# Optimization experiments

Hardware: AMD Instinct MI355X
Metric: run time of the kernel (lower is better)

## Reference

```python
import jax, jax.numpy as jnp
import numpy as np

B, C1, D1, C2, D2 = 128, 1152, 8, 10, 16
ROUTING_ITERS = 3


def squash(s, axis=-1, eps=1e-8):
    # squash(s) = (|s|^2 / (1+|s|^2)) * s / sqrt(|s|^2 + eps)
    sq = jnp.sum(s * s, axis=axis, keepdims=True)
    return (sq / (1.0 + sq)) * s / jnp.sqrt(sq + eps)


def setup_inputs() -> dict:
    key = jax.random.key(0)
    k1, k2, k3 = jax.random.split(key, 3)
    inputs = jax.random.normal(k1, (B, C1 * D1), dtype=jnp.float32)
    # W: (caps1, caps2, d2, d1), truncated normal stddev=0.1 (leading batch-1 dim dropped)
    W = jax.random.truncated_normal(k2, -2.0, 2.0, (C1, C2, D2, D1), dtype=jnp.float32) * 0.1
    # routing bias: (1, 1, caps2, d2)
    bias = jax.random.normal(k3, (1, 1, C2, D2), dtype=jnp.float32) * 0.1
    return {"inputs": inputs, "W": W, "bias": bias}


def reference(inputs, W, bias):
    b = inputs.shape[0]
    # PrimaryCaps: reshape to [B, C1, D1] then squash over the capsule dim (axis=-2 of
    # the original [B, C1, 1, D1, 1] tensor == D1 here)
    prim = squash(inputs.reshape(b, C1, D1), axis=-1)
    # DigitalCaps (fast): u_hat[b,i,j,:] = W[i,j] @ prim[b,i]  -> [B, C1, C2, D2]
    u_hat = jnp.einsum('cjdk,bck->bcjd', W, prim)
    u_stop = jax.lax.stop_gradient(u_hat)
    raw = jnp.zeros((b, C1, C2, 1), dtype=inputs.dtype)
    v = None
    for r in range(ROUTING_ITERS):
        u = u_hat if r == ROUTING_ITERS - 1 else u_stop
        c = jax.nn.softmax(raw, axis=2)                      # softmax over output caps
        s = jnp.sum(c * u, axis=1, keepdims=True) + bias     # [B, 1, C2, D2]
        v = squash(s, axis=-1)                               # squash over D2 (orig axis=-2)
        if r != ROUTING_ITERS - 1:
            # agreement: sum over D2 of u * v (v broadcasts over C1)
            raw = raw + jnp.sum(u * v, axis=-1, keepdims=True)
    # original returns [B, 1, C2, D2, 1]
    return v[..., None]
```

## Files before the change

### kernel.cpp

```cpp
#include <hip/hip_runtime.h>
#include <hip/hip_fp16.h>

#define BATCH 128
#define NC1   1152
#define ND1   8
#define NC2   10
#define ND2   16
#define SDIM  (NC2 * ND2)

#define CB 16
#define BB 32

#define NQ   6
#define QCAP (NC1 / NQ)
#define CPGP (QCAP / 32)

__device__ __forceinline__ unsigned pack_h2(float a, float b) {
    __half2 h = __floats2half2_rn(a, b);
    return *reinterpret_cast<unsigned*>(&h);
}
__device__ __forceinline__ float2 unpack_h2(unsigned v) {
    __half2 h = *reinterpret_cast<__half2*>(&v);
    return __half22float2(h);
}
__device__ __forceinline__ unsigned pmul_h2(unsigned a, unsigned b) {
    __half2 ha = *reinterpret_cast<__half2*>(&a);
    __half2 hb = *reinterpret_cast<__half2*>(&b);
    __half2 r = __hmul2(ha, hb);
    return *reinterpret_cast<unsigned*>(&r);
}
__device__ __forceinline__ unsigned padd_h2(unsigned a, unsigned b) {
    __half2 ha = *reinterpret_cast<__half2*>(&a);
    __half2 hb = *reinterpret_cast<__half2*>(&b);
    __half2 r = __hadd2(ha, hb);
    return *reinterpret_cast<unsigned*>(&r);
}

template<int CTRL>
__device__ __forceinline__ unsigned dpp_mov(unsigned v) {
    return (unsigned)__builtin_amdgcn_mov_dpp((int)v, CTRL, 0xF, 0xF, true);
}
__device__ __forceinline__ unsigned row_reduce_h2(unsigned t2) {
    t2 = padd_h2(t2, dpp_mov<0x128>(t2));
    t2 = padd_h2(t2, dpp_mov<0x124>(t2));
    t2 = padd_h2(t2, dpp_mov<0x122>(t2));
    t2 = padd_h2(t2, dpp_mov<0x121>(t2));
    return t2;
}

__global__ void caps_zero(float* __restrict__ s0) {
    s0[blockIdx.x * 256 + threadIdx.x] = 0.0f;
}

template<int JP0, int NJP>
__device__ __forceinline__ void uhat_half(
    const float* __restrict__ W, unsigned* __restrict__ u_ws,
    float* __restrict__ s0, const float (*prim)[CB][ND1],
    int cb, int bb, int c_glob, int cl, int d, int wl)
{
    float w[NJP][2][8];
    #pragma unroll
    for (int t = 0; t < NJP; ++t) {
        #pragma unroll
        for (int jj = 0; jj < 2; ++jj) {
            const int j = 2 * (JP0 + t) + jj;
            const float* Wr = W + (((size_t)c_glob * NC2 + j) * ND2 + d) * ND1;
            float4 w0 = *(const float4*)(Wr);
            float4 w1 = *(const float4*)(Wr + 4);
            w[t][jj][0] = w0.x; w[t][jj][1] = w0.y;
            w[t][jj][2] = w0.z; w[t][jj][3] = w0.w;
            w[t][jj][4] = w1.x; w[t][jj][5] = w1.y;
            w[t][jj][6] = w1.z; w[t][jj][7] = w1.w;
        }
    }
    for (int k = 0; k < BB; ++k) {
        const int b = (k + cb) & (BB - 1);
        const int bglob = bb * BB + b;
        float p[ND1];
        #pragma unroll
        for (int kk = 0; kk < ND1; ++kk) p[kk] = prim[b][cl][kk];

        unsigned* ur = u_ws + ((size_t)bglob * 5 * NC1 + c_glob) * 16 + d;
        #pragma unroll
        for (int t = 0; t < NJP; ++t) {
            const int jp = JP0 + t;
            float u0 = 0.f, u1 = 0.f;
            #pragma unroll
            for (int kk = 0; kk < ND1; ++kk) {
                u0 += w[t][0][kk] * p[kk];
                u1 += w[t][1][kk] * p[kk];
            }
            unsigned pk = pack_h2(u0, u1);
            ur[(size_t)jp * (NC1 * 16)] = pk;
            pk = padd_h2(pk, (unsigned)__shfl_xor((int)pk, 16));
            pk = padd_h2(pk, (unsigned)__shfl_xor((int)pk, 32));
            if (wl < 16) {
                float2 f = unpack_h2(pk);
                atomicAdd(&s0[(size_t)bglob * SDIM + (2*jp)   * 16 + d], f.x);
                atomicAdd(&s0[(size_t)bglob * SDIM + (2*jp+1) * 16 + d], f.y);
            }
        }
    }
}

__global__ __launch_bounds__(256, 2) void caps_uhat(
    const float* __restrict__ x,
    const float* __restrict__ W,
    unsigned* __restrict__ u_ws,
    float* __restrict__ s0)
{
    const int cb  = blockIdx.x;
    const int bb  = blockIdx.y;
    const int tid = threadIdx.x;
    const int cl  = tid >> 4;
    const int d   = tid & 15;
    const int wl  = tid & 63;

    __shared__ float prim[BB][CB][ND1];

    for (int i = tid; i < BB * CB; i += 256) {
        const int b = i >> 4, c = i & 15;
        const float* xr = x + ((size_t)(bb * BB + b) * NC1 + (cb * CB + c)) * ND1;
        float4 a0 = *(const float4*)(xr);
        float4 a1 = *(const float4*)(xr + 4);
        float sq = a0.x*a0.x + a0.y*a0.y + a0.z*a0.z + a0.w*a0.w
                 + a1.x*a1.x + a1.y*a1.y + a1.z*a1.z + a1.w*a1.w;
        float g = (sq / (1.0f + sq)) * rsqrtf(sq + 1e-8f);
        prim[b][c][0] = a0.x * g; prim[b][c][1] = a0.y * g;
        prim[b][c][2] = a0.z * g; prim[b][c][3] = a0.w * g;
        prim[b][c][4] = a1.x * g; prim[b][c][5] = a1.y * g;
        prim[b][c][6] = a1.z * g; prim[b][c][7] = a1.w * g;
    }
    __syncthreads();

    const int c_glob = cb * CB + cl;
    uhat_half<0, 3>(W, u_ws, s0, prim, cb, bb, c_glob, cl, d, wl);
    uhat_half<3, 2>(W, u_ws, s0, prim, cb, bb, c_glob, cl, d, wl);
}

__global__ __launch_bounds__(512, 1) void caps_pass(
    const unsigned* __restrict__ u_ws,
    const float* __restrict__ s0,
    const float* __restrict__ spart_in,
    const float* __restrict__ bias,
    float* __restrict__ spart_out,
    int mode)
{
    const int bx   = blockIdx.x;
    const int b    = bx / NQ;
    const int q    = bx % NQ;
    const int tid  = threadIdx.x;
    const int grp  = tid >> 4;
    const int d    = tid & 15;
    const int wave = tid >> 6;

    __shared__ float vl[SDIM];
    __shared__ float sred[8][SDIM];

    if (tid < SDIM) {
        float bv = bias[tid];
        float s_a = 0.1f * s0[(size_t)b * SDIM + tid] + bv;
        float qa = s_a * s_a;
        qa += __shfl_xor(qa, 1); qa += __shfl_xor(qa, 2);
        qa += __shfl_xor(qa, 4); qa += __shfl_xor(qa, 8);
        float v = (qa / (1.0f + qa)) * rsqrtf(qa + 1e-8f) * s_a;
        if (mode == 1) {
            float s_b = bv;
            #pragma unroll
            for (int qq = 0; qq < NQ; ++qq)
                s_b += spart_in[((size_t)b * NQ + qq) * SDIM + tid];
            float qb = s_b * s_b;
            qb += __shfl_xor(qb, 1); qb += __shfl_xor(qb, 2);
            qb += __shfl_xor(qb, 4); qb += __shfl_xor(qb, 8);
            v += (qb / (1.0f + qb)) * rsqrtf(qb + 1e-8f) * s_b;
        }
        vl[tid] = v;
    }
    __syncthreads();

    unsigned vsf[5];
    #pragma unroll
    for (int jp = 0; jp < 5; ++jp)
        vsf[jp] = pack_h2(vl[(2*jp)*16 + d], vl[(2*jp+1)*16 + d]);

    const unsigned* ub = u_ws + (size_t)b * 5 * NC1 * 16 + d;
    const int c0 = q * QCAP + grp;

    float sp[NC2];
    #pragma unroll
    for (int j = 0; j < NC2; ++j) sp[j] = 0.0f;

    unsigned o[5], on[5];
    #pragma unroll
    for (int jp = 0; jp < 5; ++jp)
        o[jp] = ub[(size_t)jp * (NC1 * 16) + (size_t)c0 * 16];

    for (int i = 0; i < CPGP; ++i) {
        if (i + 1 < CPGP) {
            const int c = c0 + (i + 1) * 32;
            #pragma unroll
            for (int jp = 0; jp < 5; ++jp)
                on[jp] = ub[(size_t)jp * (NC1 * 16) + (size_t)c * 16];
        }
        float u[NC2], r[NC2];
        #pragma unroll
        for (int jp = 0; jp < 5; ++jp) {
            float2 f = unpack_h2(o[jp]);
            u[2*jp] = f.x; u[2*jp+1] = f.y;
            unsigned t2 = row_reduce_h2(pmul_h2(o[jp], vsf[jp]));
            float2 rr = unpack_h2(t2);
            r[2*jp] = rr.x; r[2*jp+1] = rr.y;
        }
        float ssum = 0.0f;
        #pragma unroll
        for (int j = 0; j < NC2; ++j) { r[j] = __expf(r[j]); ssum += r[j]; }
        float inv = 1.0f / ssum;
        #pragma unroll
        for (int j = 0; j < NC2; ++j) sp[j] += (r[j] * inv) * u[j];
        #pragma unroll
        for (int jp = 0; jp < 5; ++jp) o[jp] = on[jp];
    }

    #pragma unroll
    for (int j = 0; j < NC2; ++j) {
        sp[j] += __shfl_xor(sp[j], 16);
        sp[j] += __shfl_xor(sp[j], 32);
    }
    if ((tid & 63) < 16) {
        #pragma unroll
        for (int j = 0; j < NC2; ++j) sred[wave][j * 16 + d] = sp[j];
    }
    __syncthreads();
    if (tid < SDIM) {
        float acc = 0.0f;
        #pragma unroll
        for (int w = 0; w < 8; ++w) acc += sred[w][tid];
        spart_out[((size_t)b * NQ + q) * SDIM + tid] = acc;
    }
}

__global__ void caps_comb2(const float* __restrict__ spart,
                           const float* __restrict__ bias,
                           float* __restrict__ out) {
    const int b = blockIdx.x, tid = threadIdx.x;
    if (tid >= SDIM) return;
    float s = bias[tid];
    #pragma unroll
    for (int q = 0; q < NQ; ++q)
        s += spart[((size_t)b * NQ + q) * SDIM + tid];
    float sq = s * s;
    sq += __shfl_xor(sq, 1); sq += __shfl_xor(sq, 2);
    sq += __shfl_xor(sq, 4); sq += __shfl_xor(sq, 8);
    out[(size_t)b * SDIM + tid] = (sq / (1.0f + sq)) * rsqrtf(sq + 1e-8f) * s;
}

__global__ __launch_bounds__(1024) void caps_fused(
    const float* __restrict__ x, const float* __restrict__ W,
    const float* __restrict__ bias, float* __restrict__ out)
{
    const int b    = blockIdx.x;
    const int tid  = threadIdx.x;
    const int grp  = tid >> 4;
    const int d    = tid & 15;
    const int wave = tid >> 6;
    const int lane = tid & 63;

    __shared__ float prim[NC1][ND1];
    __shared__ float sred[16][SDIM];
    __shared__ float vbuf[SDIM];

    const float* xb = x + (size_t)b * (NC1 * ND1);
    for (int c = tid; c < NC1; c += 1024) {
        float4 a0 = *(const float4*)(xb + c * 8);
        float4 a1 = *(const float4*)(xb + c * 8 + 4);
        float sq = a0.x*a0.x + a0.y*a0.y + a0.z*a0.z + a0.w*a0.w
                 + a1.x*a1.x + a1.y*a1.y + a1.z*a1.z + a1.w*a1.w;
        float g = (sq / (1.0f + sq)) * rsqrtf(sq + 1e-8f);
        prim[c][0] = a0.x * g; prim[c][1] = a0.y * g;
        prim[c][2] = a0.z * g; prim[c][3] = a0.w * g;
        prim[c][4] = a1.x * g; prim[c][5] = a1.y * g;
        prim[c][6] = a1.z * g; prim[c][7] = a1.w * g;
    }
    __syncthreads();

    float vsum[NC2], sp[NC2];
    for (int pass = 0; pass < 3; ++pass) {
        #pragma unroll
        for (int j = 0; j < NC2; ++j) sp[j] = 0.0f;
        for (int c = grp; c < NC1; c += 64) {
            float p[8];
            #pragma unroll
            for (int k = 0; k < 8; ++k) p[k] = prim[c][k];
            const float* Wc = W + (size_t)c * (NC2 * ND2 * ND1) + d * ND1;
            float u[NC2];
            #pragma unroll
            for (int j = 0; j < NC2; ++j) {
                const float4 w0 = *(const float4*)(Wc + j * (ND2 * ND1));
                const float4 w1 = *(const float4*)(Wc + j * (ND2 * ND1) + 4);
                u[j] = w0.x*p[0] + w0.y*p[1] + w0.z*p[2] + w0.w*p[3]
                     + w1.x*p[4] + w1.y*p[5] + w1.z*p[6] + w1.w*p[7];
            }
            if (pass == 0) {
                #pragma unroll
                for (int j = 0; j < NC2; ++j) sp[j] += u[j];
            } else {
                float r[NC2];
                #pragma unroll
                for (int j = 0; j < NC2; ++j) {
                    float t = u[j] * vsum[j];
                    t += __shfl_xor(t, 1); t += __shfl_xor(t, 2);
                    t += __shfl_xor(t, 4); t += __shfl_xor(t, 8);
                    r[j] = t;
                }
                float m = r[0];
                #pragma unroll
                for (int j = 1; j < NC2; ++j) m = fmaxf(m, r[j]);
                float ssum = 0.0f;
                #pragma unroll
                for (int j = 0; j < NC2; ++j) { r[j] = __expf(r[j] - m); ssum += r[j]; }
                float inv = 1.0f / ssum;
                #pragma unroll
                for (int j = 0; j < NC2; ++j) sp[j] += (r[j] * inv) * u[j];
            }
        }
        #pragma unroll
        for (int j = 0; j < NC2; ++j) {
            sp[j] += __shfl_xor(sp[j], 16);
            sp[j] += __shfl_xor(sp[j], 32);
        }
        if (lane < 16) {
            #pragma unroll
            for (int j = 0; j < NC2; ++j) sred[wave][j * 16 + d] = sp[j];
        }
        __syncthreads();
        if (tid < SDIM) {
            float acc = 0.0f;
            #pragma unroll
            for (int w = 0; w < 16; ++w) acc += sred[w][tid];
            float s = bias[tid] + (pass == 0 ? 0.1f * acc : acc);
            float sq = s * s;
            sq += __shfl_xor(sq, 1); sq += __shfl_xor(sq, 2);
            sq += __shfl_xor(sq, 4); sq += __shfl_xor(sq, 8);
            float vv = (sq / (1.0f + sq)) * rsqrtf(sq + 1e-8f) * s;
            if (pass == 2) out[(size_t)b * SDIM + tid] = vv;
            else           vbuf[tid] = vv;
        }
        __syncthreads();
        if (pass < 2) {
            #pragma unroll
            for (int j = 0; j < NC2; ++j) {
                float vv = vbuf[j * 16 + d];
                vsum[j] = (pass == 0) ? vv : (vsum[j] + vv);
            }
        }
        __syncthreads();
    }
}

extern "C" void kernel_launch(void* const* d_in, const int* in_sizes, int n_in,
                              void* d_out, int out_size, void* d_ws, size_t ws_size,
                              hipStream_t stream) {
    const float* x    = (const float*)d_in[0];
    const float* W    = (const float*)d_in[1];
    const float* bias = (const float*)d_in[2];
    float* out = (float*)d_out;

    const size_t u_bytes  = (size_t)BATCH * 5 * NC1 * 16 * 4;
    const size_t s0_bytes = (size_t)BATCH * SDIM * 4;
    const size_t sp_bytes = (size_t)BATCH * NQ * SDIM * 4;
    const size_t need = u_bytes + s0_bytes + 2 * sp_bytes;

    if (ws_size >= need) {
        unsigned* u_ws  = (unsigned*)d_ws;
        float*    s0    = (float*)((char*)d_ws + u_bytes);
        float*    sp1   = (float*)((char*)d_ws + u_bytes + s0_bytes);
        float*    sp2   = (float*)((char*)d_ws + u_bytes + s0_bytes + sp_bytes);

        caps_zero <<<80, 256, 0, stream>>>(s0);
        caps_uhat <<<dim3(NC1 / CB, BATCH / BB), 256, 0, stream>>>(x, W, u_ws, s0);
        caps_pass <<<BATCH * NQ, 512, 0, stream>>>(u_ws, s0, sp1, bias, sp1, 0);
        caps_pass <<<BATCH * NQ, 512, 0, stream>>>(u_ws, s0, sp1, bias, sp2, 1);
        caps_comb2<<<BATCH, 192, 0, stream>>>(sp2, bias, out);
    } else {
        caps_fused<<<BATCH, 1024, 0, stream>>>(x, W, bias, out);
    }
}
```

Measured before the change: 81.94 us.

## Merge uhat halves into one pass and preload all routing u_hat before squash

The u_hat kernel now loads all ten W rows into registers once and runs one batch loop instead of two half passes, with launch bounds lowered to one block per SIMD to allow the extra registers. The routing pass issues every global load of its u_hat slice (CPGP×5 values) at kernel entry, before the squash of s and the barrier, so memory latency overlaps that prologue instead of being double-buffered inside the loop. The cost is higher register pressure in both kernels, which lowers occupancy in caps_uhat and could cause spills.

Result: faster. 72.26 us (-11.8%).

```diff
diff --git a/kernel.cpp b/kernel.cpp
--- a/kernel.cpp
+++ b/kernel.cpp
@@ -52,58 +52,7 @@
     s0[blockIdx.x * 256 + threadIdx.x] = 0.0f;
 }
 
-template<int JP0, int NJP>
-__device__ __forceinline__ void uhat_half(
-    const float* __restrict__ W, unsigned* __restrict__ u_ws,
-    float* __restrict__ s0, const float (*prim)[CB][ND1],
-    int cb, int bb, int c_glob, int cl, int d, int wl)
-{
-    float w[NJP][2][8];
-    #pragma unroll
-    for (int t = 0; t < NJP; ++t) {
-        #pragma unroll
-        for (int jj = 0; jj < 2; ++jj) {
-            const int j = 2 * (JP0 + t) + jj;
-            const float* Wr = W + (((size_t)c_glob * NC2 + j) * ND2 + d) * ND1;
-            float4 w0 = *(const float4*)(Wr);
-            float4 w1 = *(const float4*)(Wr + 4);
-            w[t][jj][0] = w0.x; w[t][jj][1] = w0.y;
-            w[t][jj][2] = w0.z; w[t][jj][3] = w0.w;
-            w[t][jj][4] = w1.x; w[t][jj][5] = w1.y;
-            w[t][jj][6] = w1.z; w[t][jj][7] = w1.w;
-        }
-    }
-    for (int k = 0; k < BB; ++k) {
-        const int b = (k + cb) & (BB - 1);
-        const int bglob = bb * BB + b;
-        float p[ND1];
-        #pragma unroll
-        for (int kk = 0; kk < ND1; ++kk) p[kk] = prim[b][cl][kk];
-
-        unsigned* ur = u_ws + ((size_t)bglob * 5 * NC1 + c_glob) * 16 + d;
-        #pragma unroll
-        for (int t = 0; t < NJP; ++t) {
-            const int jp = JP0 + t;
-            float u0 = 0.f, u1 = 0.f;
-            #pragma unroll
-            for (int kk = 0; kk < ND1; ++kk) {
-                u0 += w[t][0][kk] * p[kk];
-                u1 += w[t][1][kk] * p[kk];
-            }
-            unsigned pk = pack_h2(u0, u1);
-            ur[(size_t)jp * (NC1 * 16)] = pk;
-            pk = padd_h2(pk, (unsigned)__shfl_xor((int)pk, 16));
-            pk = padd_h2(pk, (unsigned)__shfl_xor((int)pk, 32));
-            if (wl < 16) {
-                float2 f = unpack_h2(pk);
-                atomicAdd(&s0[(size_t)bglob * SDIM + (2*jp)   * 16 + d], f.x);
-                atomicAdd(&s0[(size_t)bglob * SDIM + (2*jp+1) * 16 + d], f.y);
-            }
-        }
-    }
-}
-
-__global__ __launch_bounds__(256, 2) void caps_uhat(
+__global__ __launch_bounds__(256, 1) void caps_uhat(
     const float* __restrict__ x,
     const float* __restrict__ W,
     unsigned* __restrict__ u_ws,
@@ -134,8 +83,43 @@
     __syncthreads();
 
     const int c_glob = cb * CB + cl;
-    uhat_half<0, 3>(W, u_ws, s0, prim, cb, bb, c_glob, cl, d, wl);
-    uhat_half<3, 2>(W, u_ws, s0, prim, cb, bb, c_glob, cl, d, wl);
+    float w[NC2][ND1];
+    #pragma unroll
+    for (int j = 0; j < NC2; ++j) {
+        const float* Wr = W + (((size_t)c_glob * NC2 + j) * ND2 + d) * ND1;
+        float4 w0 = *(const float4*)(Wr);
+        float4 w1 = *(const float4*)(Wr + 4);
+        w[j][0] = w0.x; w[j][1] = w0.y; w[j][2] = w0.z; w[j][3] = w0.w;
+        w[j][4] = w1.x; w[j][5] = w1.y; w[j][6] = w1.z; w[j][7] = w1.w;
+    }
+
+    for (int k = 0; k < BB; ++k) {
+        const int b = (k + cb) & (BB - 1);
+        const int bglob = bb * BB + b;
+        float p[ND1];
+        #pragma unroll
+        for (int kk = 0; kk < ND1; ++kk) p[kk] = prim[b][cl][kk];
+
+        unsigned* ur = u_ws + ((size_t)bglob * 5 * NC1 + c_glob) * 16 + d;
+        #pragma unroll
+        for (int jp = 0; jp < 5; ++jp) {
+            float u0 = 0.f, u1 = 0.f;
+            #pragma unroll
+            for (int kk = 0; kk < ND1; ++kk) {
+                u0 += w[2*jp  ][kk] * p[kk];
+                u1 += w[2*jp+1][kk] * p[kk];
+            }
+            unsigned pk = pack_h2(u0, u1);
+            ur[(size_t)jp * (NC1 * 16)] = pk;
+            pk = padd_h2(pk, (unsigned)__shfl_xor((int)pk, 16));
+            pk = padd_h2(pk, (unsigned)__shfl_xor((int)pk, 32));
+            if (wl < 16) {
+                float2 f = unpack_h2(pk);
+                atomicAdd(&s0[(size_t)bglob * SDIM + (2*jp)   * 16 + d], f.x);
+                atomicAdd(&s0[(size_t)bglob * SDIM + (2*jp+1) * 16 + d], f.y);
+            }
+        }
+    }
 }
 
 __global__ __launch_bounds__(512, 1) void caps_pass(
@@ -157,6 +141,17 @@
     __shared__ float vl[SDIM];
     __shared__ float sred[8][SDIM];
 
+    const unsigned* ub = u_ws + (size_t)b * 5 * NC1 * 16 + d;
+    const int c0 = q * QCAP + grp;
+    unsigned uo[CPGP][5];
+    #pragma unroll
+    for (int i = 0; i < CPGP; ++i) {
+        const int c = c0 + i * 32;
+        #pragma unroll
+        for (int jp = 0; jp < 5; ++jp)
+            uo[i][jp] = ub[(size_t)jp * (NC1 * 16) + (size_t)c * 16];
+    }
+
     if (tid < SDIM) {
         float bv = bias[tid];
         float s_a = 0.1f * s0[(size_t)b * SDIM + tid] + bv;
@@ -183,31 +178,18 @@
     for (int jp = 0; jp < 5; ++jp)
         vsf[jp] = pack_h2(vl[(2*jp)*16 + d], vl[(2*jp+1)*16 + d]);
 
-    const unsigned* ub = u_ws + (size_t)b * 5 * NC1 * 16 + d;
-    const int c0 = q * QCAP + grp;
-
     float sp[NC2];
     #pragma unroll
     for (int j = 0; j < NC2; ++j) sp[j] = 0.0f;
 
-    unsigned o[5], on[5];
-    #pragma unroll
-    for (int jp = 0; jp < 5; ++jp)
-        o[jp] = ub[(size_t)jp * (NC1 * 16) + (size_t)c0 * 16];
-
+    #pragma unroll
     for (int i = 0; i < CPGP; ++i) {
-        if (i + 1 < CPGP) {
-            const int c = c0 + (i + 1) * 32;
-            #pragma unroll
-            for (int jp = 0; jp < 5; ++jp)
-                on[jp] = ub[(size_t)jp * (NC1 * 16) + (size_t)c * 16];
-        }
         float u[NC2], r[NC2];
         #pragma unroll
         for (int jp = 0; jp < 5; ++jp) {
-            float2 f = unpack_h2(o[jp]);
+            float2 f = unpack_h2(uo[i][jp]);
             u[2*jp] = f.x; u[2*jp+1] = f.y;
-            unsigned t2 = row_reduce_h2(pmul_h2(o[jp], vsf[jp]));
+            unsigned t2 = row_reduce_h2(pmul_h2(uo[i][jp], vsf[jp]));
             float2 rr = unpack_h2(t2);
             r[2*jp] = rr.x; r[2*jp+1] = rr.y;
         }
@@ -217,8 +199,6 @@
         float inv = 1.0f / ssum;
         #pragma unroll
         for (int j = 0; j < NC2; ++j) sp[j] += (r[j] * inv) * u[j];
-        #pragma unroll
-        for (int jp = 0; jp < 5; ++jp) o[jp] = on[jp];
     }
 
     #pragma unroll
```
